# Kernel optimization log

Measured on AMD Instinct MI355X. Metric: run time of the kernel, lower is better.

## Reference

```python
import jax, jax.numpy as jnp
import numpy as np

N_CLASSES = 4
GAMMA = 2.0
B, C, D, H, W = 2, 4, 64, 192, 192
INF = 1e12


def setup_inputs() -> dict:
    key = jax.random.key(0)
    k1, k2 = jax.random.split(key)
    inp = jax.random.normal(k1, (B, C, D, H, W), dtype=jnp.float32)
    tgt = jax.random.randint(k2, (B, 1, D, H, W), 0, N_CLASSES, dtype=jnp.int32)
    return {"input": inp, "target": tgt}


def _boundary(m):
    # m: bool [..., H, W]. Boundary pixel = in mask but not 4-connected interior
    # (image border counts as background, matching cv2.findContours contours).
    pad = [(0, 0)] * (m.ndim - 2) + [(1, 1), (1, 1)]
    p = jnp.pad(m, pad)
    up = p[..., :-2, 1:-1]
    down = p[..., 2:, 1:-1]
    left = p[..., 1:-1, :-2]
    right = p[..., 1:-1, 2:]
    interior = m & up & down & left & right
    return m & ~interior


def _edt_slices(seeds):
    # seeds: bool [N, H, W]. Exact 2D Euclidean distance to nearest seed pixel,
    # via separable brute-force squared-distance passes (Felzenszwalb-style).
    h, w = seeds.shape[-2:]
    iw = jnp.arange(w, dtype=jnp.float32)
    cw = (iw[:, None] - iw[None, :]) ** 2          # [W, W]
    ih = jnp.arange(h, dtype=jnp.float32)
    ch = (ih[:, None] - ih[None, :]) ** 2          # [H, H]

    def one(seed):
        f = jnp.where(seed, 0.0, INF)              # [H, W]
        # pass along W: g[h, i] = min_j f[h, j] + (i - j)^2
        g = jnp.min(f[:, None, :] + cw[None, :, :], axis=-1)   # [H, W]
        # pass along H: d2[i, w] = min_h (i - h)^2 + g[h, w]
        d2 = jnp.min(ch[:, :, None] + g[None, :, :], axis=1)   # [H, W]
        return jnp.sqrt(jnp.minimum(d2, INF))
    return jax.lax.map(one, seeds)


def _weight_map(pred, tgt):
    # pred, tgt: int [B, D, H, W]. Per-slice boundary-distance weight map.
    b, d, h, w = tgt.shape
    wmap = jnp.zeros((b, d, h, w), jnp.float32)
    for c in range(1, N_CLASSES):  # class 0 is skipped by the original loop
        gc = tgt == c
        pc = pred == c
        present = jnp.any(gc, axis=(-2, -1))                   # [B, D]
        bnd = _boundary(gc)
        dist = _edt_slices(bnd.reshape(b * d, h, w)).reshape(b, d, h, w)
        err = gc != pc
        wmap = wmap + jnp.where(err & present[..., None, None], dist, 0.0)
    # slices with no GT labels but some predicted foreground get weight 10
    empty = ~jnp.any(tgt != 0, axis=(-2, -1))                  # [B, D]
    wmap = wmap + jnp.where(empty[..., None, None] & (pred != 0), 10.0, 0.0)
    # per-slice min-max normalization, then exp(w) - 1, then + 1
    mn = jnp.min(wmap, axis=(-2, -1), keepdims=True)
    mx = jnp.max(wmap, axis=(-2, -1), keepdims=True)
    wmap = (wmap - mn) / (mx - mn + 1e-6)
    return jnp.exp(wmap)  # (exp(w) - 1) + 1


def reference(input, target):
    t = target[:, 0]                                            # [B, D, H, W]
    logp = jax.nn.log_softmax(input, axis=1)                    # [B, C, D, H, W]
    logpt = jnp.take_along_axis(logp, t[:, None], axis=1)[:, 0]  # [B, D, H, W]
    pt = jax.lax.stop_gradient(jnp.exp(logpt))                  # .data in torch
    pred = jnp.argmax(input, axis=1)                            # [B, D, H, W]
    wmap = jax.lax.stop_gradient(_weight_map(pred, t))
    loss = -((1.0 - pt) ** GAMMA) * (logpt * wmap)
    return jnp.sum(loss)  # size_average=False
```

## Files before the change

### kernel.cpp

```cpp
#include <hip/hip_runtime.h>
#include <math.h>

#define Bv 2
#define Cc 4
#define Dd 64
#define Hh 192
#define Ww 192
#define HW (Hh*Ww)
#define NSLICE (Bv*Dd)
#define NVOX ((size_t)NSLICE*HW)
#define DHW (Dd*HW)

typedef unsigned long long u64;

#define MROWSTRIDE 4
#define MASKU64 ((size_t)NSLICE*3*Hh*MROWSTRIDE)

#define TROWS 4
#define TPX (TROWS*Ww)
#define MARGIN 12
#define SROWS (TROWS + 2*MARGIN)
#define SSTRIDE 5
#define NTILE (Hh/TROWS)

__global__ __launch_bounds__(256) void prep_kernel(const float* __restrict__ inp,
    const int* __restrict__ tgt, unsigned char* __restrict__ tp,
    float* __restrict__ focal, u64* __restrict__ masks,
    unsigned int* __restrict__ flags8) {
  int part  = blockIdx.x & 7;
  int slice = blockIdx.x >> 3;
  int b = slice >> 6, d = slice & 63;
  int wave = threadIdx.x >> 6, lane = threadIdx.x & 63;
  const float* c0 = inp + ((size_t)(b*Cc)*Dd + d)*HW;
  const float* c1p = c0 + DHW;
  const float* c2p = c0 + 2*DHW;
  const float* c3p = c0 + 3*DHW;
  const int*   tb = tgt + (size_t)slice*HW;
  unsigned int lbits = 0;
  __shared__ unsigned int sb;
  if (threadIdx.x == 0) sb = 0u;
  __syncthreads();

  for (int it = 0; it < 6; ++it) {
    int row = part*24 + wave*6 + it;
    int idx = row*Ww + lane*4;
    float4 x0, x1, x2, x3;
    int4 tv4 = make_int4(0,0,0,0), up4 = make_int4(-1,-1,-1,-1), dn4 = make_int4(-1,-1,-1,-1);
    if (lane < 48) {
      x0 = *(const float4*)(c0 + idx);
      x1 = *(const float4*)(c1p + idx);
      x2 = *(const float4*)(c2p + idx);
      x3 = *(const float4*)(c3p + idx);
      tv4 = *(const int4*)(tb + idx);
      if (row > 0)    up4 = *(const int4*)(tb + idx - Ww);
      if (row < Hh-1) dn4 = *(const int4*)(tb + idx + Ww);
    }
    int lf = __shfl(tv4.w, (lane-1)&63);
    int rt = __shfl(tv4.x, (lane+1)&63);
    unsigned nib1 = 0, nib2 = 0, nib3 = 0;
    if (lane < 48) {
      int tvs[4] = {tv4.x, tv4.y, tv4.z, tv4.w};
      int ups[4] = {up4.x, up4.y, up4.z, up4.w};
      int dns[4] = {dn4.x, dn4.y, dn4.z, dn4.w};
      int lfs[4] = {lf, tv4.x, tv4.y, tv4.z};
      int rts[4] = {tv4.y, tv4.z, tv4.w, rt};
      float a0[4] = {x0.x, x0.y, x0.z, x0.w};
      float a1[4] = {x1.x, x1.y, x1.z, x1.w};
      float a2[4] = {x2.x, x2.y, x2.z, x2.w};
      float a3[4] = {x3.x, x3.y, x3.z, x3.w};
      float4 fout;
      float* fo = (float*)&fout;
      unsigned pk4 = 0;
      #pragma unroll
      for (int k = 0; k < 4; ++k) {
        float xa = a0[k], xb = a1[k], xc = a2[k], xd = a3[k];
        int p = 0; float bst = xa;
        if (xb > bst) { bst = xb; p = 1; }
        if (xc > bst) { bst = xc; p = 2; }
        if (xd > bst) { bst = xd; p = 3; }
        int tv = tvs[k];
        float m = fmaxf(fmaxf(xa, xb), fmaxf(xc, xd));
        float e = expf(xa-m) + expf(xb-m) + expf(xc-m) + expf(xd-m);
        float xt = (tv==0) ? xa : (tv==1) ? xb : (tv==2) ? xc : xd;
        float logpt = xt - m - logf(e);
        float pt = expf(logpt);
        float om = 1.0f - pt;
        fo[k] = -(om*om)*logpt;
        pk4 |= (unsigned)(tv | (p << 4)) << (8*k);
        if (tv != 0) {
          lbits |= 1u << (tv-1);
          int col = lane*4 + k;
          bool interior = (row > 0) && (row < Hh-1) && (col > 0) && (col < Ww-1)
              && (ups[k]==tv) && (dns[k]==tv) && (lfs[k]==tv) && (rts[k]==tv);
          if (!interior) {
            if      (tv == 1) nib1 |= 1u << k;
            else if (tv == 2) nib2 |= 1u << k;
            else              nib3 |= 1u << k;
          }
        }
      }
      *(float4*)(focal + (size_t)slice*HW + idx) = fout;
      *(unsigned*)(tp + (size_t)slice*HW + idx) = pk4;
    }
    u64 m1 = (u64)nib1 << ((lane & 15)*4);
    u64 m2 = (u64)nib2 << ((lane & 15)*4);
    u64 m3 = (u64)nib3 << ((lane & 15)*4);
    #pragma unroll
    for (int off = 1; off < 16; off <<= 1) {
      m1 |= __shfl_xor(m1, off);
      m2 |= __shfl_xor(m2, off);
      m3 |= __shfl_xor(m3, off);
    }
    if (lane < 48 && (lane & 15) == 0) {
      int word = lane >> 4;
      size_t base = ((size_t)slice*3*Hh + row)*MROWSTRIDE + word;
      masks[base]                    = m1;
      masks[base + Hh*MROWSTRIDE]    = m2;
      masks[base + 2*Hh*MROWSTRIDE]  = m3;
    }
  }
  if (lbits) atomicOr(&sb, lbits);
  __syncthreads();
  if (threadIdx.x == 0) flags8[blockIdx.x] = sb;
}

__device__ __forceinline__ int nearest_bit_dist(u64 m0, u64 m1, u64 m2, int j) {
  int dr = 1<<20, dl = 1<<20;
  u64 r0, r1, r2;
  if (j >= 128)      { r0 = 0;  r1 = 0;  r2 = m2 & (~0ull << (j-128)); }
  else if (j >= 64)  { r0 = 0;  r1 = m1 & (~0ull << (j-64)); r2 = m2; }
  else               { r0 = m0 & (~0ull << j); r1 = m1; r2 = m2; }
  if      (r0) dr = (__ffsll((unsigned long long)r0) - 1) - j;
  else if (r1) dr = (__ffsll((unsigned long long)r1) + 63) - j;
  else if (r2) dr = (__ffsll((unsigned long long)r2) + 127) - j;
  u64 l0, l1, l2;
  if (j < 64)        { l0 = (j==63) ? m0 : (m0 & ((1ull<<(j+1))-1)); l1 = 0; l2 = 0; }
  else if (j < 128)  { l0 = m0; l1 = (j==127) ? m1 : (m1 & ((1ull<<(j-63))-1)); l2 = 0; }
  else               { l0 = m0; l1 = m1; l2 = (j==191) ? m2 : (m2 & ((1ull<<(j-127))-1)); }
  if      (l2) dl = j - (191 - __clzll((long long)l2));
  else if (l1) dl = j - (127 - __clzll((long long)l1));
  else if (l0) dl = j - (63  - __clzll((long long)l0));
  return dl < dr ? dl : dr;
}

__device__ __forceinline__ float edt_dist(const u64* __restrict__ smc,
    const u64* __restrict__ gmc, int li, int i, int j) {
  int best = 1 << 30;
  for (int dr = 0; dr <= MARGIN; ++dr) {
    if (dr*dr >= best) break;
    const u64* R = smc + (li-dr)*SSTRIDE;
    int dc = nearest_bit_dist(R[0], R[1], R[2], j);
    if (dc < (1<<20)) { int cand = dr*dr + dc*dc; if (cand < best) best = cand; }
    if (dr) {
      const u64* R2 = smc + (li+dr)*SSTRIDE;
      int dc2 = nearest_bit_dist(R2[0], R2[1], R2[2], j);
      if (dc2 < (1<<20)) { int cand = dr*dr + dc2*dc2; if (cand < best) best = cand; }
    }
  }
  for (int dr = MARGIN+1; dr < Hh; ++dr) {
    if (dr*dr >= best) break;
    int up = i - dr;
    if (up >= 0) {
      const u64* R = gmc + up*MROWSTRIDE;
      int dc = nearest_bit_dist(R[0], R[1], R[2], j);
      if (dc < (1<<20)) { int cand = dr*dr + dc*dc; if (cand < best) best = cand; }
    }
    int dn = i + dr;
    if (dn < Hh) {
      const u64* R = gmc + dn*MROWSTRIDE;
      int dc = nearest_bit_dist(R[0], R[1], R[2], j);
      if (dc < (1<<20)) { int cand = dr*dr + dc*dc; if (cand < best) best = cand; }
    }
  }
  return (best == (1 << 30)) ? 1.0e6f : sqrtf((float)best);
}

__device__ __forceinline__ void push16(unsigned short* list, unsigned* cnt,
    bool want, unsigned val) {
  u64 mask = __ballot(want);
  if (mask == 0) return;
  int lane = threadIdx.x & 63;
  int total = __popcll(mask);
  int leader = __ffsll((long long)mask) - 1;
  unsigned b = 0;
  if (lane == leader) b = atomicAdd(cnt, (unsigned)total);
  b = __shfl(b, leader);
  if (want) {
    int off = __popcll(mask & ((1ull << lane) - 1));
    list[b + off] = (unsigned short)val;
  }
}

__global__ __launch_bounds__(256) void edt_kernel(const unsigned char* __restrict__ tp,
    const u64* __restrict__ masks, const unsigned int* __restrict__ flags8,
    float* __restrict__ wmap, float* __restrict__ mmn, float* __restrict__ mxx) {
  __shared__ u64 sm[3*SROWS*SSTRIDE];
  __shared__ __align__(16) float wacc[TPX];
  __shared__ unsigned short list[TPX];
  __shared__ unsigned cnt, sfl;
  __shared__ float smn[4], smx[4];
  int tile  = blockIdx.x % NTILE;
  int slice = blockIdx.x / NTILE;
  int r0 = tile*TROWS;
  int tid = threadIdx.x;

  if (tid == 0) {
    unsigned f = 0;
    #pragma unroll
    for (int p = 0; p < 8; ++p) f |= flags8[slice*8 + p];
    sfl = f; cnt = 0u;
  }
  __syncthreads();
  unsigned fl = sfl;
  bool empty = ((fl & 7u) == 0u);

  for (int t = tid; t < 3*SROWS*3; t += 256) {
    int c = t / (SROWS*3);
    int rem = t - c*(SROWS*3);
    int sr = rem / 3, w = rem - sr*3;
    int gr = r0 - MARGIN + sr;
    sm[(c*SROWS + sr)*SSTRIDE + w] = (gr >= 0 && gr < Hh)
        ? masks[(((size_t)slice*3 + c)*Hh + gr)*MROWSTRIDE + w] : 0ull;
  }

  if (tid < 192) {
    unsigned pk = *(const unsigned*)(tp + (size_t)slice*HW + r0*Ww + tid*4);
    #pragma unroll
    for (int k = 0; k < 4; ++k) {
      int px = tid*4 + k;
      int byte = (pk >> (8*k)) & 0xff;
      int tv = byte & 15, pv = byte >> 4;
      wacc[px] = (empty && pv != 0) ? 10.0f : 0.0f;
      bool diff = (tv != pv);
      int cA, cB;
      if (tv && pv) { cA = tv; cB = pv; } else { cA = tv | pv; cB = 0; }
      int rl = px / Ww, j = px - rl*Ww;
      push16(list, &cnt, diff,
             (unsigned)j | ((unsigned)rl << 8) | ((unsigned)cA << 10) | ((unsigned)cB << 12));
    }
  }
  __syncthreads();

  unsigned n = cnt;
  const u64* gm0 = masks + (size_t)slice*3*Hh*MROWSTRIDE;
  for (unsigned kk = tid; kk < n; kk += 256) {
    unsigned item = list[kk];
    int j  = item & 255;
    int rl = (item >> 8) & 3;
    int cA = (item >> 10) & 3;
    int cB = (item >> 12) & 3;
    int i  = r0 + rl;
    int li = MARGIN + rl;
    float sum = 0.0f;
    if (cA && ((fl >> (cA-1)) & 1u))
      sum += edt_dist(sm + (cA-1)*SROWS*SSTRIDE, gm0 + (size_t)(cA-1)*Hh*MROWSTRIDE, li, i, j);
    if (cB && ((fl >> (cB-1)) & 1u))
      sum += edt_dist(sm + (cB-1)*SROWS*SSTRIDE, gm0 + (size_t)(cB-1)*Hh*MROWSTRIDE, li, i, j);
    wacc[rl*Ww + j] += sum;
  }
  __syncthreads();

  float lmn = 1.0e30f, lmx = 0.0f;
  if (tid < 192) {
    float4 wv = *(const float4*)&wacc[tid*4];
    lmn = fminf(fminf(wv.x, wv.y), fminf(wv.z, wv.w));
    lmx = fmaxf(fmaxf(wv.x, wv.y), fmaxf(wv.z, wv.w));
    *(float4*)(wmap + (size_t)slice*HW + r0*Ww + tid*4) = wv;
  }
  for (int off = 32; off; off >>= 1) {
    lmn = fminf(lmn, __shfl_xor(lmn, off));
    lmx = fmaxf(lmx, __shfl_xor(lmx, off));
  }
  int wid = tid >> 6;
  if ((tid & 63) == 0) { smn[wid] = lmn; smx[wid] = lmx; }
  __syncthreads();
  if (tid == 0) {
    lmn = fminf(fminf(smn[0], smn[1]), fminf(smn[2], smn[3]));
    lmx = fmaxf(fmaxf(smx[0], smx[1]), fmaxf(smx[2], smx[3]));
    mmn[blockIdx.x] = lmn;
    mxx[blockIdx.x] = lmx;
  }
}

__global__ __launch_bounds__(256) void loss_kernel(const float* __restrict__ focal,
    const float* __restrict__ wmap, const float* __restrict__ mmn,
    const float* __restrict__ mxx, float* __restrict__ pp) {
  int part  = blockIdx.x % 9;
  int slice = blockIdx.x / 9;
  __shared__ float smm[2];
  if (threadIdx.x < 64) {
    float a = (threadIdx.x < NTILE) ? mmn[slice*NTILE + threadIdx.x] : 1.0e30f;
    float c = (threadIdx.x < NTILE) ? mxx[slice*NTILE + threadIdx.x] : 0.0f;
    for (int off = 32; off; off >>= 1) {
      a = fminf(a, __shfl_xor(a, off));
      c = fmaxf(c, __shfl_xor(c, off));
    }
    if (threadIdx.x == 0) { smm[0] = a; smm[1] = c; }
  }
  __syncthreads();
  float mn = smm[0], mx = smm[1];
  float inv = 1.0f/(mx - mn + 1e-6f);
  float acc = 0.0f;
  for (int it = 0; it < 4; ++it) {
    int idx = part*4096 + it*1024 + threadIdx.x*4;
    float4 f = *(const float4*)(focal + (size_t)slice*HW + idx);
    float4 w = *(const float4*)(wmap + (size_t)slice*HW + idx);
    acc += f.x * expf((w.x-mn)*inv);
    acc += f.y * expf((w.y-mn)*inv);
    acc += f.z * expf((w.z-mn)*inv);
    acc += f.w * expf((w.w-mn)*inv);
  }
  for (int off = 32; off; off >>= 1) acc += __shfl_xor(acc, off);
  __shared__ float sa[4];
  int wid = threadIdx.x >> 6;
  if ((threadIdx.x & 63) == 0) sa[wid] = acc;
  __syncthreads();
  if (threadIdx.x == 0) pp[blockIdx.x] = sa[0]+sa[1]+sa[2]+sa[3];
}

__global__ __launch_bounds__(256) void final_kernel(const float* __restrict__ pp,
    float* __restrict__ out) {
  float acc = 0.0f;
  for (int i = threadIdx.x; i < NSLICE*9; i += 256) acc += pp[i];
  for (int off = 32; off; off >>= 1) acc += __shfl_xor(acc, off);
  __shared__ float sa[4];
  int wid = threadIdx.x >> 6;
  if ((threadIdx.x & 63) == 0) sa[wid] = acc;
  __syncthreads();
  if (threadIdx.x == 0) out[0] = sa[0]+sa[1]+sa[2]+sa[3];
}

extern "C" void kernel_launch(void* const* d_in, const int* in_sizes, int n_in,
                              void* d_out, int out_size, void* d_ws, size_t ws_size,
                              hipStream_t stream) {
  const float* inp = (const float*)d_in[0];
  const int*   tgt = (const int*)d_in[1];
  char* ws = (char*)d_ws;
  unsigned char* tp    = (unsigned char*)ws;
  float*         focal = (float*)(ws + NVOX);
  float*         wmap  = (float*)(ws + 5*NVOX);
  u64*           masks = (u64*)(ws + 9*NVOX);
  unsigned int*  flags8 = (unsigned int*)(ws + 9*NVOX + MASKU64*8);
  float*         mmn   = (float*)(flags8 + NSLICE*8);
  float*         mxx   = mmn + NSLICE*48;
  float*         pp    = mxx + NSLICE*48;

  prep_kernel<<<NSLICE*8, 256, 0, stream>>>(inp, tgt, tp, focal, masks, flags8);
  edt_kernel<<<NSLICE*NTILE, 256, 0, stream>>>(tp, masks, flags8, wmap, mmn, mxx);
  loss_kernel<<<NSLICE*9, 256, 0, stream>>>(focal, wmap, mmn, mxx, pp);
  final_kernel<<<1, 256, 0, stream>>>(pp, (float*)d_out);
}
```

Baseline: 219.7 us.

## Precompute per-row horizontal nearest-seed distances in LDS and enlarge EDT tiles

Each EDT block now covers 16 rows instead of 4 and first builds a shared byte table holding, for every row in the tile plus an 8-row margin, the horizontal distance to the nearest boundary pixel. The near-field vertical search then reads one byte per row instead of rerunning bit-scan logic for every queried pixel. The ballot-based compaction list of mismatched pixels is dropped: each thread walks pixels directly and writes the weight map and min/max without an LDS accumulator. This trades extra up-front table-building work and more branch divergence for cheaper per-query searches, a smaller margin, and fewer blocks and partial min/max entries.

After: 238.1 us. 1.08x slower.

```diff
diff --git a/kernel.cpp b/kernel.cpp
--- a/kernel.cpp
+++ b/kernel.cpp
@@ -16,12 +16,11 @@
 #define MROWSTRIDE 4
 #define MASKU64 ((size_t)NSLICE*3*Hh*MROWSTRIDE)
 
-#define TROWS 4
-#define TPX (TROWS*Ww)
-#define MARGIN 12
-#define SROWS (TROWS + 2*MARGIN)
-#define SSTRIDE 5
+#define TROWS 16
+#define MARGIN 8
+#define SR (TROWS + 2*MARGIN)
 #define NTILE (Hh/TROWS)
+#define GSTR32 52
 
 __global__ __launch_bounds__(256) void prep_kernel(const float* __restrict__ inp,
     const int* __restrict__ tgt, unsigned char* __restrict__ tp,
@@ -143,61 +142,45 @@
   return dl < dr ? dl : dr;
 }
 
-__device__ __forceinline__ float edt_dist(const u64* __restrict__ smc,
+__device__ __forceinline__ float edt_search(const unsigned char* __restrict__ gc,
     const u64* __restrict__ gmc, int li, int i, int j) {
   int best = 1 << 30;
+  #pragma unroll 4
   for (int dr = 0; dr <= MARGIN; ++dr) {
     if (dr*dr >= best) break;
-    const u64* R = smc + (li-dr)*SSTRIDE;
-    int dc = nearest_bit_dist(R[0], R[1], R[2], j);
-    if (dc < (1<<20)) { int cand = dr*dr + dc*dc; if (cand < best) best = cand; }
+    int gu = gc[(li-dr)*208 + j];
+    if (gu != 255) { int cand = dr*dr + gu*gu; if (cand < best) best = cand; }
     if (dr) {
-      const u64* R2 = smc + (li+dr)*SSTRIDE;
-      int dc2 = nearest_bit_dist(R2[0], R2[1], R2[2], j);
-      if (dc2 < (1<<20)) { int cand = dr*dr + dc2*dc2; if (cand < best) best = cand; }
-    }
-  }
-  for (int dr = MARGIN+1; dr < Hh; ++dr) {
-    if (dr*dr >= best) break;
-    int up = i - dr;
-    if (up >= 0) {
-      const u64* R = gmc + up*MROWSTRIDE;
-      int dc = nearest_bit_dist(R[0], R[1], R[2], j);
-      if (dc < (1<<20)) { int cand = dr*dr + dc*dc; if (cand < best) best = cand; }
-    }
-    int dn = i + dr;
-    if (dn < Hh) {
-      const u64* R = gmc + dn*MROWSTRIDE;
-      int dc = nearest_bit_dist(R[0], R[1], R[2], j);
-      if (dc < (1<<20)) { int cand = dr*dr + dc*dc; if (cand < best) best = cand; }
+      int gd = gc[(li+dr)*208 + j];
+      if (gd != 255) { int cand = dr*dr + gd*gd; if (cand < best) best = cand; }
+    }
+  }
+  if ((MARGIN+1)*(MARGIN+1) < best) {
+    for (int dr = MARGIN+1; dr < Hh; ++dr) {
+      if (dr*dr >= best) break;
+      int up = i - dr;
+      if (up >= 0) {
+        const u64* R = gmc + up*MROWSTRIDE;
+        int dc = nearest_bit_dist(R[0], R[1], R[2], j);
+        if (dc < (1<<20)) { int cand = dr*dr + dc*dc; if (cand < best) best = cand; }
+      }
+      int dn = i + dr;
+      if (dn < Hh) {
+        const u64* R = gmc + dn*MROWSTRIDE;
+        int dc = nearest_bit_dist(R[0], R[1], R[2], j);
+        if (dc < (1<<20)) { int cand = dr*dr + dc*dc; if (cand < best) best = cand; }
+      }
     }
   }
   return (best == (1 << 30)) ? 1.0e6f : sqrtf((float)best);
-}
-
-__device__ __forceinline__ void push16(unsigned short* list, unsigned* cnt,
-    bool want, unsigned val) {
-  u64 mask = __ballot(want);
-  if (mask == 0) return;
-  int lane = threadIdx.x & 63;
-  int total = __popcll(mask);
-  int leader = __ffsll((long long)mask) - 1;
-  unsigned b = 0;
-  if (lane == leader) b = atomicAdd(cnt, (unsigned)total);
-  b = __shfl(b, leader);
-  if (want) {
-    int off = __popcll(mask & ((1ull << lane) - 1));
-    list[b + off] = (unsigned short)val;
-  }
 }
 
 __global__ __launch_bounds__(256) void edt_kernel(const unsigned char* __restrict__ tp,
     const u64* __restrict__ masks, const unsigned int* __restrict__ flags8,
     float* __restrict__ wmap, float* __restrict__ mmn, float* __restrict__ mxx) {
-  __shared__ u64 sm[3*SROWS*SSTRIDE];
-  __shared__ __align__(16) float wacc[TPX];
-  __shared__ unsigned short list[TPX];
-  __shared__ unsigned cnt, sfl;
+  __shared__ u64 smask[3*SR*3];
+  __shared__ unsigned g32[3*SR*GSTR32];
+  __shared__ unsigned sfl;
   __shared__ float smn[4], smx[4];
   int tile  = blockIdx.x % NTILE;
   int slice = blockIdx.x / NTILE;
@@ -208,64 +191,59 @@
     unsigned f = 0;
     #pragma unroll
     for (int p = 0; p < 8; ++p) f |= flags8[slice*8 + p];
-    sfl = f; cnt = 0u;
-  }
-  __syncthreads();
+    sfl = f;
+  }
+  for (int t = tid; t < 3*SR*3; t += 256) {
+    int c = t / (SR*3);
+    int rem = t - c*(SR*3);
+    int sr = rem / 3, w = rem - sr*3;
+    int gr = r0 - MARGIN + sr;
+    smask[t] = (gr >= 0 && gr < Hh)
+        ? masks[(((size_t)slice*3 + c)*Hh + gr)*MROWSTRIDE + w] : 0ull;
+  }
+  __syncthreads();
+
+  for (int t = tid; t < 3*SR*48; t += 256) {
+    int c = t / (SR*48);
+    int rem = t - c*(SR*48);
+    int sr = rem / 48, jw = rem - sr*48;
+    const u64* M = &smask[(c*SR + sr)*3];
+    u64 m0 = M[0], m1 = M[1], m2 = M[2];
+    unsigned pack = 0;
+    #pragma unroll
+    for (int k = 0; k < 4; ++k) {
+      int dd = nearest_bit_dist(m0, m1, m2, jw*4 + k);
+      if (dd > 255) dd = 255;
+      pack |= (unsigned)dd << (8*k);
+    }
+    g32[(c*SR + sr)*GSTR32 + jw] = pack;
+  }
+  __syncthreads();
+
   unsigned fl = sfl;
   bool empty = ((fl & 7u) == 0u);
-
-  for (int t = tid; t < 3*SROWS*3; t += 256) {
-    int c = t / (SROWS*3);
-    int rem = t - c*(SROWS*3);
-    int sr = rem / 3, w = rem - sr*3;
-    int gr = r0 - MARGIN + sr;
-    sm[(c*SROWS + sr)*SSTRIDE + w] = (gr >= 0 && gr < Hh)
-        ? masks[(((size_t)slice*3 + c)*Hh + gr)*MROWSTRIDE + w] : 0ull;
-  }
-
-  if (tid < 192) {
-    unsigned pk = *(const unsigned*)(tp + (size_t)slice*HW + r0*Ww + tid*4);
-    #pragma unroll
-    for (int k = 0; k < 4; ++k) {
-      int px = tid*4 + k;
-      int byte = (pk >> (8*k)) & 0xff;
-      int tv = byte & 15, pv = byte >> 4;
-      wacc[px] = (empty && pv != 0) ? 10.0f : 0.0f;
-      bool diff = (tv != pv);
+  const unsigned char* g8 = (const unsigned char*)g32;
+  const u64* gmbase = masks + (size_t)slice*3*Hh*MROWSTRIDE;
+
+  float lmn = 1.0e30f, lmx = 0.0f;
+  for (int k = 0; k < (TROWS*Ww)/256; ++k) {
+    int lpx = k*256 + tid;
+    int rl = lpx / Ww, j = lpx - rl*Ww;
+    int i = r0 + rl;
+    int li = MARGIN + rl;
+    int byte = tp[(size_t)slice*HW + r0*Ww + lpx];
+    int tv = byte & 15, pv = byte >> 4;
+    float w = (empty && pv != 0) ? 10.0f : 0.0f;
+    if (tv != pv) {
       int cA, cB;
       if (tv && pv) { cA = tv; cB = pv; } else { cA = tv | pv; cB = 0; }
-      int rl = px / Ww, j = px - rl*Ww;
-      push16(list, &cnt, diff,
-             (unsigned)j | ((unsigned)rl << 8) | ((unsigned)cA << 10) | ((unsigned)cB << 12));
-    }
-  }
-  __syncthreads();
-
-  unsigned n = cnt;
-  const u64* gm0 = masks + (size_t)slice*3*Hh*MROWSTRIDE;
-  for (unsigned kk = tid; kk < n; kk += 256) {
-    unsigned item = list[kk];
-    int j  = item & 255;
-    int rl = (item >> 8) & 3;
-    int cA = (item >> 10) & 3;
-    int cB = (item >> 12) & 3;
-    int i  = r0 + rl;
-    int li = MARGIN + rl;
-    float sum = 0.0f;
-    if (cA && ((fl >> (cA-1)) & 1u))
-      sum += edt_dist(sm + (cA-1)*SROWS*SSTRIDE, gm0 + (size_t)(cA-1)*Hh*MROWSTRIDE, li, i, j);
-    if (cB && ((fl >> (cB-1)) & 1u))
-      sum += edt_dist(sm + (cB-1)*SROWS*SSTRIDE, gm0 + (size_t)(cB-1)*Hh*MROWSTRIDE, li, i, j);
-    wacc[rl*Ww + j] += sum;
-  }
-  __syncthreads();
-
-  float lmn = 1.0e30f, lmx = 0.0f;
-  if (tid < 192) {
-    float4 wv = *(const float4*)&wacc[tid*4];
-    lmn = fminf(fminf(wv.x, wv.y), fminf(wv.z, wv.w));
-    lmx = fmaxf(fmaxf(wv.x, wv.y), fmaxf(wv.z, wv.w));
-    *(float4*)(wmap + (size_t)slice*HW + r0*Ww + tid*4) = wv;
+      if ((fl >> (cA-1)) & 1u)
+        w += edt_search(g8 + (cA-1)*SR*208, gmbase + (size_t)(cA-1)*Hh*MROWSTRIDE, li, i, j);
+      if (cB && ((fl >> (cB-1)) & 1u))
+        w += edt_search(g8 + (cB-1)*SR*208, gmbase + (size_t)(cB-1)*Hh*MROWSTRIDE, li, i, j);
+    }
+    wmap[(size_t)slice*HW + r0*Ww + lpx] = w;
+    lmn = fminf(lmn, w); lmx = fmaxf(lmx, w);
   }
   for (int off = 32; off; off >>= 1) {
     lmn = fminf(lmn, __shfl_xor(lmn, off));
@@ -342,8 +320,8 @@
   u64*           masks = (u64*)(ws + 9*NVOX);
   unsigned int*  flags8 = (unsigned int*)(ws + 9*NVOX + MASKU64*8);
   float*         mmn   = (float*)(flags8 + NSLICE*8);
-  float*         mxx   = mmn + NSLICE*48;
-  float*         pp    = mxx + NSLICE*48;
+  float*         mxx   = mmn + NSLICE*NTILE;
+  float*         pp    = mxx + NSLICE*NTILE;
 
   prep_kernel<<<NSLICE*8, 256, 0, stream>>>(inp, tgt, tp, focal, masks, flags8);
   edt_kernel<<<NSLICE*NTILE, 256, 0, stream>>>(tp, masks, flags8, wmap, mmn, mxx);
```
